# Performance work log

Measured on AMD Instinct MI355X. Metric: run time of the kernel, lower is better.

The kernel has to match this reference:

```python
import jax, jax.numpy as jnp
import numpy as np

N, E = 100000, 1600000
D_IN, D_H, D_OUT = 512, 256, 32
ALPHA, K = 0.1, 10


def setup_inputs() -> dict:
    key = jax.random.key(0)
    ks = jax.random.split(key, 8)
    feats = jax.random.normal(ks[0], (N, D_IN), dtype=jnp.float32)
    src = jax.random.randint(ks[1], (E,), 0, N, dtype=jnp.int32)
    dst = jax.random.randint(ks[2], (E,), 0, N, dtype=jnp.int32)
    s1 = 1.0 / np.sqrt(D_IN)
    s2 = 1.0 / np.sqrt(D_H)
    W1 = jax.random.uniform(ks[3], (D_IN, D_H), jnp.float32, -s1, s1)
    b1 = jax.random.uniform(ks[4], (D_H,), jnp.float32, -s1, s1)
    W2 = jax.random.uniform(ks[5], (D_H, D_OUT), jnp.float32, -s2, s2)
    b2 = jax.random.uniform(ks[6], (D_OUT,), jnp.float32, -s2, s2)
    return {"feats": feats, "src": src, "dst": dst,
            "W1": W1, "b1": b1, "W2": W2, "b2": b2}


def reference(feats, src, dst, W1, b1, W2, b2):
    # MLP stack (num_layers=2, norm_type='none', activation=relu, dropout=eval/no-op)
    h = feats @ W1 + b1            # [N, D_H]
    h1 = h                          # h_list entry (pre-norm/activation)
    h = jax.nn.relu(h)
    h = h @ W2 + b2                 # [N, D_OUT]

    # APPNPConv: symmetric degree normalization (DGL: clamp degree min 1)
    ones_e = jnp.ones((src.shape[0],), dtype=h.dtype)
    deg_out = jax.ops.segment_sum(ones_e, src, num_segments=N)
    deg_in = jax.ops.segment_sum(ones_e, dst, num_segments=N)
    norm_src = jnp.power(jnp.clip(deg_out, 1.0), -0.5)[:, None]  # [N,1]
    norm_dst = jnp.power(jnp.clip(deg_in, 1.0), -0.5)[:, None]   # [N,1]

    h0 = h
    for _ in range(K):  # fixed small K, unrolled hops
        msg = (h * norm_src)[src]                                  # gather [E, D_OUT]
        agg = jax.ops.segment_sum(msg, dst, num_segments=N)        # scatter-add
        h = (1.0 - ALPHA) * (agg * norm_dst) + ALPHA * h0
    return (h1, h)
```

## Files before the change

### kernel.cpp

```cpp
#include <hip/hip_runtime.h>

#define NN 100000
#define EE 1600000
#define DIN 512
#define DH 256
#define DOUT 32
#define RANKB 512
#define HNR 25
#define HNS 16
#define RBH 4000
#define HES 100000
#define HISTB (HNR*HNS)

typedef _Float16 h16x8 __attribute__((ext_vector_type(8)));
typedef _Float16 h16x4 __attribute__((ext_vector_type(4)));
typedef float f32x4 __attribute__((ext_vector_type(4)));

union HU { unsigned int u; _Float16 h[2]; };

__global__ __launch_bounds__(256) void conv_w1(const float* __restrict__ W1, _Float16* __restrict__ W1T){
  int i = blockIdx.x*256 + threadIdx.x;
  if (i < DIN*DH){
    int c = i >> 9, k = i & 511;
    W1T[i] = (_Float16)W1[k*DH + c];
  }
}
__global__ __launch_bounds__(256) void conv_w2(const float* __restrict__ W2, _Float16* __restrict__ W2T){
  int i = blockIdx.x*256 + threadIdx.x;
  if (i < DH*DOUT){
    int c = i >> 8, k = i & 255;
    W2T[i] = (_Float16)W2[k*DOUT + c];
  }
}

__global__ __launch_bounds__(256) void gemm1_deg(
    const float* __restrict__ feats, const _Float16* __restrict__ W1T,
    const float* __restrict__ b1, float* __restrict__ h1,
    const int* __restrict__ src, const int* __restrict__ dst,
    int* __restrict__ cnt, int* __restrict__ pO, int* __restrict__ rnk)
{
  __shared__ __align__(16) int smem[RBH];
  const int bid = blockIdx.x;
  const int tid = threadIdx.x;

  if (bid < RANKB){
    for (int i = bid*256 + tid; i < EE; i += RANKB*256)
      rnk[i] = atomicAdd(&cnt[dst[i]], 1);
    return;
  }
  if (bid < RANKB + HISTB){
    const int hb = bid - RANKB;
    const int r = hb / HNS, s = hb % HNS;
    const int r0 = r * RBH;
    for (int j = tid; j < RBH; j += 256) smem[j] = 0;
    __syncthreads();
    const int4* s4 = reinterpret_cast<const int4*>(src + (size_t)s*HES);
    for (int i = tid; i < HES/8; i += 256){
      int4 a = s4[2*i], b = s4[2*i+1];
      int k;
      k = a.x - r0; if ((unsigned)k < RBH) atomicAdd(&smem[k], 1);
      k = a.y - r0; if ((unsigned)k < RBH) atomicAdd(&smem[k], 1);
      k = a.z - r0; if ((unsigned)k < RBH) atomicAdd(&smem[k], 1);
      k = a.w - r0; if ((unsigned)k < RBH) atomicAdd(&smem[k], 1);
      k = b.x - r0; if ((unsigned)k < RBH) atomicAdd(&smem[k], 1);
      k = b.y - r0; if ((unsigned)k < RBH) atomicAdd(&smem[k], 1);
      k = b.z - r0; if ((unsigned)k < RBH) atomicAdd(&smem[k], 1);
      k = b.w - r0; if ((unsigned)k < RBH) atomicAdd(&smem[k], 1);
    }
    __syncthreads();
    for (int j = tid; j < RBH; j += 256) pO[(size_t)s*NN + r0 + j] = smem[j];
    return;
  }

  _Float16 (*At)[40] = reinterpret_cast<_Float16(*)[40]>(smem);
  _Float16 (*Bt)[40] = reinterpret_cast<_Float16(*)[40]>(reinterpret_cast<char*>(smem) + 5120);
  const int gid  = bid - (RANKB + HISTB);
  const int col0 = (gid & 1) * 128;
  const int row0 = (gid >> 1) * 64;

  const int lane = tid & 63, wave = tid >> 6;
  const int wr = wave >> 1, wc = wave & 1;
  const int l15 = lane & 15, kg = lane >> 4;
  const int arow = tid >> 2, aseg = (tid & 3) * 8;
  const int bcol = tid >> 1, bseg = (tid & 1) * 16;
  const bool aok = (row0 + arow) < NN;
  const float* aP = feats + (size_t)(row0+arow)*DIN + aseg;
  const _Float16* bP = W1T + (size_t)(col0+bcol)*DIN + bseg;

  f32x4 acc[2][4];
#pragma unroll
  for (int m=0;m<2;m++)
#pragma unroll
    for (int n=0;n<4;n++){ acc[m][n][0]=0.f; acc[m][n][1]=0.f; acc[m][n][2]=0.f; acc[m][n][3]=0.f; }

  float4 fa0 = make_float4(0,0,0,0), fa1 = make_float4(0,0,0,0);
  h16x8 fb0, fb1;
  if (aok){
    fa0 = *reinterpret_cast<const float4*>(aP);
    fa1 = *reinterpret_cast<const float4*>(aP + 4);
  }
  fb0 = *reinterpret_cast<const h16x8*>(bP);
  fb1 = *reinterpret_cast<const h16x8*>(bP + 8);

  for (int t=0; t<16; ++t){
    {
      h16x4 v0, v1;
      v0[0]=(_Float16)fa0.x; v0[1]=(_Float16)fa0.y; v0[2]=(_Float16)fa0.z; v0[3]=(_Float16)fa0.w;
      v1[0]=(_Float16)fa1.x; v1[1]=(_Float16)fa1.y; v1[2]=(_Float16)fa1.z; v1[3]=(_Float16)fa1.w;
      *reinterpret_cast<h16x4*>(&At[arow][aseg])   = v0;
      *reinterpret_cast<h16x4*>(&At[arow][aseg+4]) = v1;
      *reinterpret_cast<h16x8*>(&Bt[bcol][bseg])   = fb0;
      *reinterpret_cast<h16x8*>(&Bt[bcol][bseg+8]) = fb1;
    }
    __syncthreads();
    if (t < 15){
      int k0 = (t+1)*32;
      if (aok){
        fa0 = *reinterpret_cast<const float4*>(aP + k0);
        fa1 = *reinterpret_cast<const float4*>(aP + k0 + 4);
      }
      fb0 = *reinterpret_cast<const h16x8*>(bP + k0);
      fb1 = *reinterpret_cast<const h16x8*>(bP + k0 + 8);
    }
    h16x8 af[2], bfr[4];
#pragma unroll
    for (int m=0;m<2;m++) af[m]  = *reinterpret_cast<const h16x8*>(&At[wr*32 + m*16 + l15][kg*8]);
#pragma unroll
    for (int n=0;n<4;n++) bfr[n] = *reinterpret_cast<const h16x8*>(&Bt[wc*64 + n*16 + l15][kg*8]);
#pragma unroll
    for (int m=0;m<2;m++)
#pragma unroll
      for (int n=0;n<4;n++)
        acc[m][n] = __builtin_amdgcn_mfma_f32_16x16x32_f16(af[m], bfr[n], acc[m][n], 0, 0, 0);
    __syncthreads();
  }
  const int rb = kg*4;
#pragma unroll
  for (int n=0;n<4;n++){
    int col = col0 + wc*64 + n*16 + l15;
    float bias = b1[col];
#pragma unroll
    for (int m=0;m<2;m++){
#pragma unroll
      for (int j=0;j<4;j++){
        int g = row0 + wr*32 + m*16 + rb + j;
        if (g < NN) h1[(size_t)g*DH + col] = acc[m][n][j] + bias;
      }
    }
  }
}

__global__ __launch_bounds__(256) void combine(
    const int* __restrict__ pO, const int* __restrict__ cnt,
    int* __restrict__ degI, float* __restrict__ nS, float* __restrict__ nD)
{
  int v = blockIdx.x*256 + threadIdx.x;
  if (v >= NN) return;
  int so = 0;
#pragma unroll
  for (int s=0;s<HNS;s++) so += pO[(size_t)s*NN + v];
  int si = cnt[v];
  degI[v] = si;
  nS[v] = rsqrtf((float)(so > 0 ? so : 1));
  nD[v] = rsqrtf((float)(si > 0 ? si : 1));
}

__global__ __launch_bounds__(1024) void scan1(const int* __restrict__ degI, int* __restrict__ offs, int* __restrict__ bsum){
  __shared__ int sm[1024];
  int t = threadIdx.x;
  int g = blockIdx.x*1024 + t;
  int v = (g < NN) ? degI[g] : 0;
  sm[t] = v; __syncthreads();
  for (int o=1;o<1024;o<<=1){
    int a = (t>=o)? sm[t-o] : 0;
    __syncthreads();
    sm[t] += a;
    __syncthreads();
  }
  if (g < NN) offs[g] = sm[t] - v;
  if (t == 1023) bsum[blockIdx.x] = sm[t];
}
__global__ __launch_bounds__(128) void scan2(const int* __restrict__ bsum, int* __restrict__ boff, int nb){
  __shared__ int sm[128];
  int t = threadIdx.x;
  int v = (t < nb)? bsum[t] : 0;
  sm[t] = v; __syncthreads();
  for (int o=1;o<128;o<<=1){
    int a = (t>=o)? sm[t-o] : 0;
    __syncthreads();
    sm[t] += a;
    __syncthreads();
  }
  if (t < nb) boff[t] = sm[t] - v;
}
__global__ __launch_bounds__(256) void scan3(int* __restrict__ offs, const int* __restrict__ boff){
  int i = blockIdx.x*256 + threadIdx.x;
  if (i < NN) offs[i] += boff[i >> 10];
}

__global__ __launch_bounds__(256) void fused2(
    const float* __restrict__ h1, const _Float16* __restrict__ W2T,
    const float* __restrict__ b2, const float* __restrict__ nS,
    _Float16* __restrict__ h0h, _Float16* __restrict__ hsh,
    const int* __restrict__ src, const int* __restrict__ dst,
    const int* __restrict__ offs, const int* __restrict__ rnk,
    int* __restrict__ csrc)
{
  const int bid = blockIdx.x;
  const int tid = threadIdx.x;
  if (bid < 1024){
    for (int i = bid*256 + tid; i < EE; i += 1024*256){
      csrc[offs[dst[i]] + rnk[i]] = src[i];
    }
    return;
  }
  const int gid = bid - 1024;
  const int row0 = gid * 256;
  const int lane = tid & 63, wave = tid >> 6;
  const int l15 = lane & 15, kg = lane >> 4;

  f32x4 acc[4][2];
#pragma unroll
  for (int m=0;m<4;m++)
#pragma unroll
    for (int n=0;n<2;n++){ acc[m][n][0]=0.f; acc[m][n][1]=0.f; acc[m][n][2]=0.f; acc[m][n][3]=0.f; }

  const float* aP[4]; bool aok[4];
#pragma unroll
  for (int m=0;m<4;m++){
    int r = row0 + wave*64 + m*16 + l15;
    aok[m] = (r < NN);
    aP[m] = h1 + (size_t)r*DH + kg*8;
  }
  const _Float16* bP[2];
#pragma unroll
  for (int n=0;n<2;n++)
    bP[n] = W2T + (size_t)(n*16 + l15)*DH + kg*8;

  for (int t=0; t<8; ++t){
    const int k0 = t*32;
    h16x8 bf[2], af[4];
#pragma unroll
    for (int n=0;n<2;n++) bf[n] = *reinterpret_cast<const h16x8*>(bP[n] + k0);
#pragma unroll
    for (int m=0;m<4;m++){
      float4 x = make_float4(0,0,0,0), y = make_float4(0,0,0,0);
      if (aok[m]){
        x = *reinterpret_cast<const float4*>(aP[m] + k0);
        y = *reinterpret_cast<const float4*>(aP[m] + k0 + 4);
      }
      h16x8 v;
      v[0]=(_Float16)fmaxf(x.x,0.f); v[1]=(_Float16)fmaxf(x.y,0.f);
      v[2]=(_Float16)fmaxf(x.z,0.f); v[3]=(_Float16)fmaxf(x.w,0.f);
      v[4]=(_Float16)fmaxf(y.x,0.f); v[5]=(_Float16)fmaxf(y.y,0.f);
      v[6]=(_Float16)fmaxf(y.z,0.f); v[7]=(_Float16)fmaxf(y.w,0.f);
      af[m] = v;
    }
#pragma unroll
    for (int m=0;m<4;m++)
#pragma unroll
      for (int n=0;n<2;n++)
        acc[m][n] = __builtin_amdgcn_mfma_f32_16x16x32_f16(af[m], bf[n], acc[m][n], 0, 0, 0);
  }
  const int rb = kg*4;
#pragma unroll
  for (int n=0;n<2;n++){
    int col = n*16 + l15;
    float bias = b2[col];
#pragma unroll
    for (int m=0;m<4;m++){
#pragma unroll
      for (int j=0;j<4;j++){
        int g = row0 + wave*64 + m*16 + rb + j;
        if (g < NN){
          float val = acc[m][n][j] + bias;
          h0h[(size_t)g*DOUT + col] = (_Float16)val;
          hsh[(size_t)g*DOUT + col] = (_Float16)(nS[g] * val);
        }
      }
    }
  }
}

template<bool LAST>
__global__ __launch_bounds__(256) void propC(
    const uint4* __restrict__ hs, const uint4* __restrict__ h0,
    uint4* __restrict__ hs_out, float4* __restrict__ out4,
    const int* __restrict__ offs, const int* __restrict__ degI,
    const int* __restrict__ csrc,
    const float* __restrict__ nS, const float* __restrict__ nD)
{
  const int nw = gridDim.x * 4;
  const int wid = (blockIdx.x*256 + threadIdx.x) >> 6;
  const int lane = threadIdx.x & 63;
  const int n = lane >> 4;
  const int s = (lane >> 2) & 3;
  const int q = lane & 3;

  const int NQ = (NN + 3) / 4;
  for (int vq = wid; vq < NQ; vq += nw){
    const int v = vq*4 + n;
    const bool vok = (v < NN);
    int beg = 0, cnt = 0;
    if (vok){ beg = offs[v]; cnt = degI[v]; }
    float a[8];
#pragma unroll
    for (int k=0;k<8;k++) a[k]=0.f;

    int i = s;
    int e = (i < cnt) ? csrc[beg + i] : -1;
    while (__any(e >= 0)){
      int i2 = i + 4;
      int e2 = (i2 < cnt) ? csrc[beg + i2] : -1;
      if (e >= 0){
        uint4 p = hs[(size_t)e*4 + q];
        HU u0,u1,u2,u3; u0.u=p.x; u1.u=p.y; u2.u=p.z; u3.u=p.w;
        a[0]+=(float)u0.h[0]; a[1]+=(float)u0.h[1];
        a[2]+=(float)u1.h[0]; a[3]+=(float)u1.h[1];
        a[4]+=(float)u2.h[0]; a[5]+=(float)u2.h[1];
        a[6]+=(float)u3.h[0]; a[7]+=(float)u3.h[1];
      }
      e = e2; i = i2;
    }
#pragma unroll
    for (int k=0;k<8;k++){
      a[k] += __shfl_xor(a[k], 4);
      a[k] += __shfl_xor(a[k], 8);
    }
    if (s == 0 && vok){
      float nd = nD[v];
      uint4 hp = h0[(size_t)v*4 + q];
      HU u0,u1,u2,u3; u0.u=hp.x; u1.u=hp.y; u2.u=hp.z; u3.u=hp.w;
      float r[8];
      r[0]=0.9f*nd*a[0]+0.1f*(float)u0.h[0]; r[1]=0.9f*nd*a[1]+0.1f*(float)u0.h[1];
      r[2]=0.9f*nd*a[2]+0.1f*(float)u1.h[0]; r[3]=0.9f*nd*a[3]+0.1f*(float)u1.h[1];
      r[4]=0.9f*nd*a[4]+0.1f*(float)u2.h[0]; r[5]=0.9f*nd*a[5]+0.1f*(float)u2.h[1];
      r[6]=0.9f*nd*a[6]+0.1f*(float)u3.h[0]; r[7]=0.9f*nd*a[7]+0.1f*(float)u3.h[1];
      if (LAST){
        out4[(size_t)v*8 + q*2]     = make_float4(r[0],r[1],r[2],r[3]);
        out4[(size_t)v*8 + q*2 + 1] = make_float4(r[4],r[5],r[6],r[7]);
      } else {
        float ns = nS[v];
        HU o0,o1,o2,o3;
        o0.h[0]=(_Float16)(ns*r[0]); o0.h[1]=(_Float16)(ns*r[1]);
        o1.h[0]=(_Float16)(ns*r[2]); o1.h[1]=(_Float16)(ns*r[3]);
        o2.h[0]=(_Float16)(ns*r[4]); o2.h[1]=(_Float16)(ns*r[5]);
        o3.h[0]=(_Float16)(ns*r[6]); o3.h[1]=(_Float16)(ns*r[7]);
        uint4 o; o.x=o0.u; o.y=o1.u; o.z=o2.u; o.w=o3.u;
        hs_out[(size_t)v*4 + q] = o;
      }
    }
  }
}

extern "C" void kernel_launch(void* const* d_in, const int* in_sizes, int n_in,
                              void* d_out, int out_size, void* d_ws, size_t ws_size,
                              hipStream_t stream)
{
  const float* feats = (const float*)d_in[0];
  const int*   src   = (const int*)d_in[1];
  const int*   dst   = (const int*)d_in[2];
  const float* W1    = (const float*)d_in[3];
  const float* b1    = (const float*)d_in[4];
  const float* W2    = (const float*)d_in[5];
  const float* b2    = (const float*)d_in[6];
  float* out = (float*)d_out;

  char* ws = (char*)d_ws;
  size_t off = 0;
  auto alloc = [&](size_t bytes) -> void* {
    void* p = ws + off;
    off = (off + bytes + 255) & ~(size_t)255;
    return p;
  };
  _Float16* W1T = (_Float16*)alloc((size_t)DIN*DH*2);
  _Float16* W2T = (_Float16*)alloc((size_t)DH*DOUT*2);
  int*   cnt    = (int*)  alloc((size_t)NN*4);
  int*   pO     = (int*)  alloc((size_t)HNS*NN*4);
  int*   degI   = (int*)  alloc((size_t)NN*4);
  float* nS     = (float*)alloc((size_t)NN*4);
  float* nD     = (float*)alloc((size_t)NN*4);
  int*   offs   = (int*)  alloc((size_t)NN*4);
  int*   bsum   = (int*)  alloc(512);
  int*   boff   = (int*)  alloc(512);
  int*   rnk    = (int*)  alloc((size_t)EE*4);
  int*   csrc   = (int*)  alloc((size_t)EE*4);
  _Float16* h0h = (_Float16*)alloc((size_t)NN*DOUT*2);
  _Float16* hs0 = (_Float16*)alloc((size_t)NN*DOUT*2);
  unsigned int* pA = (unsigned int*)alloc((size_t)NN*DOUT*2);
  unsigned int* pB = (unsigned int*)alloc((size_t)NN*DOUT*2);

  hipMemsetAsync(cnt, 0, (size_t)NN*4, stream);

  conv_w1<<<(DIN*DH+255)/256, 256, 0, stream>>>(W1, W1T);
  conv_w2<<<(DH*DOUT+255)/256, 256, 0, stream>>>(W2, W2T);

  gemm1_deg<<<RANKB + HISTB + 2*((NN+63)/64), 256, 0, stream>>>(
      feats, W1T, b1, out, src, dst, cnt, pO, rnk);

  combine<<<(NN+255)/256, 256, 0, stream>>>(pO, cnt, degI, nS, nD);
  int nb = (NN+1023)/1024;
  scan1<<<nb, 1024, 0, stream>>>(degI, offs, bsum);
  scan2<<<1, 128, 0, stream>>>(bsum, boff, nb);
  scan3<<<(NN+255)/256, 256, 0, stream>>>(offs, boff);

  fused2<<<1024 + (NN+255)/256, 256, 0, stream>>>(out, W2T, b2, nS, h0h, hs0,
                                                  src, dst, offs, rnk, csrc);

  float4* out4 = (float4*)(out + (size_t)NN*DH);
  const uint4* cur = (const uint4*)hs0;
  const uint4* h0u = (const uint4*)h0h;
  for (int it=0; it<9; ++it){
    uint4* nxt = (uint4*)((it&1)? pB : pA);
    propC<false><<<3125, 256, 0, stream>>>(cur, h0u, nxt, nullptr, offs, degI, csrc, nS, nD);
    cur = nxt;
  }
  propC<true><<<3125, 256, 0, stream>>>(cur, h0u, nullptr, out4, offs, degI, csrc, nS, nD);
}
```

Before: 512.8 us.

## Build CSR via partitioned shared-memory histograms instead of global atomic ranks

Replaces the global atomicAdd rank computation on in-degree counters with the same range-partitioned shared-memory histogram scheme already used for out-degree, applied to dst. Combine turns the per-slice partial counts into exclusive per-slice offsets, and the CSR fill uses per-block shared-memory cursors seeded from those offsets, so the rank array, its memset and the global atomics go away. In exchange every fill block rescans its whole 100K-edge slice and keeps only the dst values in its range, which multiplies edge reads, and the order of neighbours within a row is no longer deterministic.

```diff
diff --git a/kernel.cpp b/kernel.cpp
--- a/kernel.cpp
+++ b/kernel.cpp
@@ -5,7 +5,6 @@
 #define DIN 512
 #define DH 256
 #define DOUT 32
-#define RANKB 512
 #define HNR 25
 #define HNS 16
 #define RBH 4000
@@ -33,28 +32,25 @@
   }
 }
 
-__global__ __launch_bounds__(256) void gemm1_deg(
+__global__ __launch_bounds__(256) void gemm1_hist(
     const float* __restrict__ feats, const _Float16* __restrict__ W1T,
     const float* __restrict__ b1, float* __restrict__ h1,
     const int* __restrict__ src, const int* __restrict__ dst,
-    int* __restrict__ cnt, int* __restrict__ pO, int* __restrict__ rnk)
+    int* __restrict__ pO, int* __restrict__ pI)
 {
   __shared__ __align__(16) int smem[RBH];
   const int bid = blockIdx.x;
   const int tid = threadIdx.x;
 
-  if (bid < RANKB){
-    for (int i = bid*256 + tid; i < EE; i += RANKB*256)
-      rnk[i] = atomicAdd(&cnt[dst[i]], 1);
-    return;
-  }
-  if (bid < RANKB + HISTB){
-    const int hb = bid - RANKB;
+  if (bid < 2*HISTB){
+    const int hb = (bid < HISTB) ? bid : bid - HISTB;
+    const int* keys = (bid < HISTB) ? src : dst;
+    int* part = (bid < HISTB) ? pO : pI;
     const int r = hb / HNS, s = hb % HNS;
     const int r0 = r * RBH;
     for (int j = tid; j < RBH; j += 256) smem[j] = 0;
     __syncthreads();
-    const int4* s4 = reinterpret_cast<const int4*>(src + (size_t)s*HES);
+    const int4* s4 = reinterpret_cast<const int4*>(keys + (size_t)s*HES);
     for (int i = tid; i < HES/8; i += 256){
       int4 a = s4[2*i], b = s4[2*i+1];
       int k;
@@ -68,13 +64,13 @@
       k = b.w - r0; if ((unsigned)k < RBH) atomicAdd(&smem[k], 1);
     }
     __syncthreads();
-    for (int j = tid; j < RBH; j += 256) pO[(size_t)s*NN + r0 + j] = smem[j];
+    for (int j = tid; j < RBH; j += 256) part[(size_t)s*NN + r0 + j] = smem[j];
     return;
   }
 
   _Float16 (*At)[40] = reinterpret_cast<_Float16(*)[40]>(smem);
   _Float16 (*Bt)[40] = reinterpret_cast<_Float16(*)[40]>(reinterpret_cast<char*>(smem) + 5120);
-  const int gid  = bid - (RANKB + HISTB);
+  const int gid  = bid - 2*HISTB;
   const int col0 = (gid & 1) * 128;
   const int row0 = (gid >> 1) * 64;
 
@@ -151,7 +147,7 @@
 }
 
 __global__ __launch_bounds__(256) void combine(
-    const int* __restrict__ pO, const int* __restrict__ cnt,
+    const int* __restrict__ pO, int* __restrict__ pI,
     int* __restrict__ degI, float* __restrict__ nS, float* __restrict__ nD)
 {
   int v = blockIdx.x*256 + threadIdx.x;
@@ -159,7 +155,13 @@
   int so = 0;
 #pragma unroll
   for (int s=0;s<HNS;s++) so += pO[(size_t)s*NN + v];
-  int si = cnt[v];
+  int si = 0;
+#pragma unroll
+  for (int s=0;s<HNS;s++){
+    int c = pI[(size_t)s*NN + v];
+    pI[(size_t)s*NN + v] = si;
+    si += c;
+  }
   degI[v] = si;
   nS[v] = rsqrtf((float)(so > 0 ? so : 1));
   nD[v] = rsqrtf((float)(si > 0 ? si : 1));
@@ -203,18 +205,29 @@
     const float* __restrict__ b2, const float* __restrict__ nS,
     _Float16* __restrict__ h0h, _Float16* __restrict__ hsh,
     const int* __restrict__ src, const int* __restrict__ dst,
-    const int* __restrict__ offs, const int* __restrict__ rnk,
+    const int* __restrict__ pI, const int* __restrict__ offs,
     int* __restrict__ csrc)
 {
+  __shared__ int cur[RBH];
   const int bid = blockIdx.x;
   const int tid = threadIdx.x;
-  if (bid < 1024){
-    for (int i = bid*256 + tid; i < EE; i += 1024*256){
-      csrc[offs[dst[i]] + rnk[i]] = src[i];
+  if (bid < HISTB){
+    const int r = bid / HNS, s = bid % HNS;
+    const int r0 = r * RBH;
+    for (int j = tid; j < RBH; j += 256)
+      cur[j] = pI[(size_t)s*NN + r0 + j] + offs[r0 + j];
+    __syncthreads();
+    const int e0 = s * HES, e1 = e0 + HES;
+    for (int i = e0 + tid; i < e1; i += 256){
+      int d = dst[i] - r0;
+      if ((unsigned)d < RBH){
+        int pos = atomicAdd(&cur[d], 1);
+        csrc[pos] = src[i];
+      }
     }
     return;
   }
-  const int gid = bid - 1024;
+  const int gid = bid - HISTB;
   const int row0 = gid * 256;
   const int lane = tid & 63, wave = tid >> 6;
   const int l15 = lane & 15, kg = lane >> 4;
@@ -375,37 +388,34 @@
   };
   _Float16* W1T = (_Float16*)alloc((size_t)DIN*DH*2);
   _Float16* W2T = (_Float16*)alloc((size_t)DH*DOUT*2);
-  int*   cnt    = (int*)  alloc((size_t)NN*4);
   int*   pO     = (int*)  alloc((size_t)HNS*NN*4);
+  int*   pI     = (int*)  alloc((size_t)HNS*NN*4);
   int*   degI   = (int*)  alloc((size_t)NN*4);
   float* nS     = (float*)alloc((size_t)NN*4);
   float* nD     = (float*)alloc((size_t)NN*4);
   int*   offs   = (int*)  alloc((size_t)NN*4);
   int*   bsum   = (int*)  alloc(512);
   int*   boff   = (int*)  alloc(512);
-  int*   rnk    = (int*)  alloc((size_t)EE*4);
   int*   csrc   = (int*)  alloc((size_t)EE*4);
   _Float16* h0h = (_Float16*)alloc((size_t)NN*DOUT*2);
   _Float16* hs0 = (_Float16*)alloc((size_t)NN*DOUT*2);
   unsigned int* pA = (unsigned int*)alloc((size_t)NN*DOUT*2);
   unsigned int* pB = (unsigned int*)alloc((size_t)NN*DOUT*2);
 
-  hipMemsetAsync(cnt, 0, (size_t)NN*4, stream);
-
   conv_w1<<<(DIN*DH+255)/256, 256, 0, stream>>>(W1, W1T);
   conv_w2<<<(DH*DOUT+255)/256, 256, 0, stream>>>(W2, W2T);
 
-  gemm1_deg<<<RANKB + HISTB + 2*((NN+63)/64), 256, 0, stream>>>(
-      feats, W1T, b1, out, src, dst, cnt, pO, rnk);
-
-  combine<<<(NN+255)/256, 256, 0, stream>>>(pO, cnt, degI, nS, nD);
+  gemm1_hist<<<2*HISTB + 2*((NN+63)/64), 256, 0, stream>>>(
+      feats, W1T, b1, out, src, dst, pO, pI);
+
+  combine<<<(NN+255)/256, 256, 0, stream>>>(pO, pI, degI, nS, nD);
   int nb = (NN+1023)/1024;
   scan1<<<nb, 1024, 0, stream>>>(degI, offs, bsum);
   scan2<<<1, 128, 0, stream>>>(bsum, boff, nb);
   scan3<<<(NN+255)/256, 256, 0, stream>>>(offs, boff);
 
-  fused2<<<1024 + (NN+255)/256, 256, 0, stream>>>(out, W2T, b2, nS, h0h, hs0,
-                                                  src, dst, offs, rnk, csrc);
+  fused2<<<HISTB + (NN+255)/256, 256, 0, stream>>>(out, W2T, b2, nS, h0h, hs0,
+                                                   src, dst, pI, offs, csrc);
 
   float4* out4 = (float4*)(out + (size_t)NN*DH);
   const uint4* cur = (const uint4*)hs0;
```

Result: slower. 645.3 us (+25.8%).
